# Performance work log

Hardware: AMD Instinct MI355X
Metric: run time of the kernel (lower is better)

The kernel has to match this reference:

```python
import jax, jax.numpy as jnp
import numpy as np
import math

T = 120      # frame_num == audio_len == max_seq_len
D = 64       # hidden_layer_size
H = 2        # n_head
DH = D // H
DFF = 2 * D
DOUT = 31
PERIOD = 10
EPS = 1e-5
NEG = -1e9
SCALE = 1.0 / math.sqrt(DH)
SLOPES = (1.0 / 16.0, 1.0 / 256.0)  # ALiBi slopes for n_head=2


def _pe():
    # PeriodicPositionalEncoding: sinusoid over one period, tiled
    pos = jnp.arange(PERIOD, dtype=jnp.float32)[:, None]
    div = jnp.exp(jnp.arange(0, D, 2, dtype=jnp.float32) * (-math.log(10000.0) / D))
    s, c = jnp.sin(pos * div), jnp.cos(pos * div)
    pe = jnp.stack([s, c], axis=-1).reshape(PERIOD, D)  # interleave sin/cos
    return jnp.tile(pe, (T // PERIOD + 1, 1))[:T]


def _alibi_mask():
    # causal mask + ALiBi bias: alibi[i,j] = -slope * floor((i-j)/period) for j<=i
    slopes = jnp.array(SLOPES, dtype=jnp.float32)
    i = jnp.arange(T)[:, None]
    j = jnp.arange(T)[None, :]
    rel = ((i - j) // PERIOD).astype(jnp.float32)
    return jnp.where(j <= i, -slopes[:, None, None] * rel, NEG)  # [H,T,T]


def _ln(x, g, b):
    m = x.mean(-1, keepdims=True)
    v = ((x - m) ** 2).mean(-1, keepdims=True)
    return (x - m) / jnp.sqrt(v + EPS) * g + b


def setup_inputs() -> dict:
    key = jax.random.key(0)
    ks = iter(jax.random.split(key, 32))
    n = lambda shape, s=0.05: jax.random.normal(next(ks), shape, dtype=jnp.float32) * s
    inp = {
        'audio': jax.random.normal(next(ks), (1, T, 1024), dtype=jnp.float32),
        'W_audio': n((D, 1024)), 'b_audio': n((D,)),
        'obj_W': n((D, 5)),
        'Wq': n((D, D)), 'bq': n((D,)), 'Wk': n((D, D)), 'bk': n((D,)),
        'Wv': n((D, D)), 'bv': n((D,)), 'Wo': n((D, D)), 'bo': n((D,)),
        'Wv2': n((D, D)), 'bv2': n((D,)), 'Wo2': n((D, D)), 'bo2': n((D,)),
        'g1': jnp.ones((D,)), 'be1': jnp.zeros((D,)),
        'g2': jnp.ones((D,)), 'be2': jnp.zeros((D,)),
        'g3': jnp.ones((D,)), 'be3': jnp.zeros((D,)),
        'W1': n((DFF, D)), 'c1': n((DFF,)), 'W2': n((D, DFF)), 'c2': n((D,)),
        'Wr': n((DOUT, D)), 'br': n((DOUT,)), 'Wm': n((D, DOUT)), 'bm': n((D,)),
    }
    return inp


def _forward(audio, W_audio, b_audio, obj_W, Wq, bq, Wk, bk, Wv, bv, Wo, bo,
             Wv2, bv2, Wo2, bo2, g1, be1, g2, be2, g3, be3,
             W1, c1, W2, c2, Wr, br, Wm, bm):
    mem = audio[0] @ W_audio.T + b_audio          # [S,D], S == T
    style = obj_W[:, 0]                            # obj_vector @ [1,0,0,0,0]
    pe = _pe()
    mask = _alibi_mask()
    slopes = jnp.array(SLOPES, dtype=jnp.float32)
    jarr = jnp.arange(T)

    # enc_dec_mask leaves exactly one memory key per target row (anti-diagonal
    # from the end); the feedback row t at step t always attends memory[-1],
    # so its cross-attn output is just the projected value of the last frame.
    cross_last = (mem[-1] @ Wv2.T + bv2) @ Wo2.T + bo2  # [D]

    def step(emb, t):
        # decode only the last row (row t) of the growing sequence; 1-layer
        # post-norm decoder => row t depends only on input rows 0..t.
        x = emb + pe                                 # PPE over prefix
        xq = jnp.take(x, t, axis=0)                  # [D]
        q = (xq @ Wq.T + bq).reshape(H, DH)
        k = (x @ Wk.T + bk).reshape(T, H, DH)
        v = (x @ Wv.T + bv).reshape(T, H, DH)
        bias = jnp.where(jarr <= t,
                         -slopes[:, None] * ((t - jarr) // PERIOD).astype(jnp.float32),
                         NEG)                        # [H,T]
        sc = jnp.einsum('hd,shd->hs', q, k) * SCALE + bias
        a = jax.nn.softmax(sc, axis=-1)
        sa = jnp.einsum('hs,shd->hd', a, v).reshape(D) @ Wo.T + bo
        h1 = _ln(xq + sa, g1, be1)
        h2 = _ln(h1 + cross_last, g2, be2)
        h3 = _ln(h2 + jax.nn.relu(h2 @ W1.T + c1) @ W2.T + c2, g3, be3)
        new = (h3 @ Wr.T + br) @ Wm.T + bm + style   # vertice_map(vertice_map_r(.)) + style
        emb = jax.lax.dynamic_update_slice(emb, new[None, :], (t + 1, 0))
        return emb, None

    emb0 = jnp.zeros((T, D), audio.dtype).at[0].set(style)
    emb, _ = jax.lax.scan(step, emb0, jnp.arange(T - 1))

    # final full-length decode (last loop iteration of the torch module)
    x = emb + pe
    q = (x @ Wq.T + bq).reshape(T, H, DH)
    k = (x @ Wk.T + bk).reshape(T, H, DH)
    v = (x @ Wv.T + bv).reshape(T, H, DH)
    sc = jnp.einsum('thd,shd->hts', q, k) * SCALE + mask
    a = jax.nn.softmax(sc, axis=-1)
    sa = jnp.einsum('hts,shd->thd', a, v).reshape(T, D) @ Wo.T + bo
    h1 = _ln(x + sa, g1, be1)
    # at length T with S == T the enc_dec_mask aligns target row j <-> memory row j
    cross = (mem @ Wv2.T + bv2) @ Wo2.T + bo2
    h2 = _ln(h1 + cross, g2, be2)
    h3 = _ln(h2 + jax.nn.relu(h2 @ W1.T + c1) @ W2.T + c2, g3, be3)
    return (h3 @ Wr.T + br)[None]                    # [1,T,31]


def reference(audio, W_audio, b_audio, obj_W, Wq, bq, Wk, bk, Wv, bv, Wo, bo,
              Wv2, bv2, Wo2, bo2, g1, be1, g2, be2, g3, be3,
              W1, c1, W2, c2, Wr, br, Wm, bm):
    return _forward(audio, W_audio, b_audio, obj_W, Wq, bq, Wk, bk, Wv, bv, Wo, bo,
                    Wv2, bv2, Wo2, bo2, g1, be1, g2, be2, g3, be3,
                    W1, c1, W2, c2, Wr, br, Wm, bm)
```

## Files before the change

kernel.cpp:

```cpp
#include <hip/hip_runtime.h>

typedef unsigned short u16;
typedef unsigned int   u32;
typedef _Float16 f16;
typedef f16 h2 __attribute__((ext_vector_type(2)));
typedef f16 h4 __attribute__((ext_vector_type(4)));
typedef f16 h8 __attribute__((ext_vector_type(8)));

#define T_    120
#define D_    64
#define DOUT_ 31
#define KROW_ 68
#define VROW_ 132
#define EROW_ 68

#if defined(__has_builtin)
#if __has_builtin(__builtin_amdgcn_fdot2)
#define DOT2(a,b,c) __builtin_amdgcn_fdot2((a),(b),(c),false)
#endif
#endif
#ifndef DOT2
#define DOT2(a,b,c) ((float)(a).x*(float)(b).x + ((float)(a).y*(float)(b).y + (c)))
#endif
#define SHV(x,i,j) __builtin_shufflevector((x),(x),(i),(j))

__device__ __forceinline__ h2 pk(float a, float b){
#if defined(__has_builtin) && __has_builtin(__builtin_amdgcn_cvt_pkrtz)
  return __builtin_bit_cast(h2, __builtin_amdgcn_cvt_pkrtz(a, b));
#else
  h2 r; r.x = (f16)a; r.y = (f16)b; return r;
#endif
}
__device__ __forceinline__ u16 f2h16(float x){
  f16 v = (f16)x; u16 r; __builtin_memcpy(&r, &v, 2); return r;
}
__device__ __forceinline__ float fast_rcp(float x){
#if defined(__has_builtin) && __has_builtin(__builtin_amdgcn_rcpf)
  return __builtin_amdgcn_rcpf(x);
#else
  return 1.f / x;
#endif
}
#define WSYNC() do{ __asm__ __volatile__("" ::: "memory"); __builtin_amdgcn_wave_barrier(); }while(0)

__device__ __forceinline__ float dpp_sum(float x){
  int t;
  t = __builtin_amdgcn_update_dpp(0, __float_as_int(x), 0x111, 0xf, 0xf, true); x += __int_as_float(t);
  t = __builtin_amdgcn_update_dpp(0, __float_as_int(x), 0x112, 0xf, 0xf, true); x += __int_as_float(t);
  t = __builtin_amdgcn_update_dpp(0, __float_as_int(x), 0x114, 0xf, 0xf, true); x += __int_as_float(t);
  t = __builtin_amdgcn_update_dpp(0, __float_as_int(x), 0x118, 0xf, 0xf, true); x += __int_as_float(t);
  t = __builtin_amdgcn_update_dpp(0, __float_as_int(x), 0x142, 0xf, 0xf, true); x += __int_as_float(t);
  t = __builtin_amdgcn_update_dpp(0, __float_as_int(x), 0x143, 0xf, 0xf, true); x += __int_as_float(t);
  return __int_as_float(__builtin_amdgcn_readlane(__float_as_int(x), 63));
}
__device__ __forceinline__ float dpp_max_pos(float x){
  int t;
  t = __builtin_amdgcn_update_dpp(0, __float_as_int(x), 0x111, 0xf, 0xf, true); x = fmaxf(x, __int_as_float(t));
  t = __builtin_amdgcn_update_dpp(0, __float_as_int(x), 0x112, 0xf, 0xf, true); x = fmaxf(x, __int_as_float(t));
  t = __builtin_amdgcn_update_dpp(0, __float_as_int(x), 0x114, 0xf, 0xf, true); x = fmaxf(x, __int_as_float(t));
  t = __builtin_amdgcn_update_dpp(0, __float_as_int(x), 0x118, 0xf, 0xf, true); x = fmaxf(x, __int_as_float(t));
  t = __builtin_amdgcn_update_dpp(0, __float_as_int(x), 0x142, 0xf, 0xf, true); x = fmaxf(x, __int_as_float(t));
  t = __builtin_amdgcn_update_dpp(0, __float_as_int(x), 0x143, 0xf, 0xf, true); x = fmaxf(x, __int_as_float(t));
  return __int_as_float(__builtin_amdgcn_readlane(__float_as_int(x), 63));
}
__device__ __forceinline__ float pe_val(int row, int i){
  const float coef = -0.28782313662425574f;
  int p = row % 10;
  float dv  = __expf((float)(i >> 1) * coef);
  float ang = (float)p * dv;
  return (i & 1) ? __cosf(ang) : __sinf(ang);
}
__device__ __forceinline__ void loadrow32(h2* dst, const float* row){
  #pragma unroll
  for (int r = 0; r < 16; ++r){
    float4 f = ((const float4*)row)[r];
    dst[2*r]   = pk(f.x, f.y);
    dst[2*r+1] = pk(f.z, f.w);
  }
}

__global__ __launch_bounds__(128, 1) void k_scan(
    const float* __restrict__ audio,
    const float* __restrict__ Wa, const float* __restrict__ ba,
    const float* __restrict__ Wv2, const float* __restrict__ bv2,
    const float* __restrict__ Wo2, const float* __restrict__ bo2,
    const float* __restrict__ objW,
    const float* __restrict__ Wq, const float* __restrict__ bq,
    const float* __restrict__ Wk, const float* __restrict__ bk,
    const float* __restrict__ Wv, const float* __restrict__ bv,
    const float* __restrict__ Wo, const float* __restrict__ bo,
    const float* __restrict__ g1, const float* __restrict__ be1,
    const float* __restrict__ g2, const float* __restrict__ be2,
    const float* __restrict__ g3, const float* __restrict__ be3,
    const float* __restrict__ W1, const float* __restrict__ c1,
    const float* __restrict__ W2, const float* __restrict__ c2,
    const float* __restrict__ Wm, const float* __restrict__ br,
    const float* __restrict__ bm, const float* __restrict__ Wr,
    u16* __restrict__ xw16, u16* __restrict__ Kw16, u16* __restrict__ Vw16)
{
  __shared__ __align__(16) f16 KcS[128*KROW_];
  __shared__ __align__(16) f16 VcS[D_*VROW_];
  __shared__ __align__(16) f16 xwS[T_*D_];
  __shared__ __align__(16) f16 EcS[64*EROW_];
  __shared__ __align__(16) f16 sch[256];
  __shared__ __align__(16) f16 xh[64], qh[64], h2h[64], h3h[64];
  __shared__ __align__(16) f16 at2h[64];
  __shared__ __align__(16) f16 fsh[128];
  __shared__ float pP0[64], pP1[64];
  __shared__ float ivP[2];
  __shared__ float pe_tab[640];

  const int tid = threadIdx.x;
  const int i = tid & 63;
  const int hh = tid >> 6;
  const bool w1w = hh != 0;

  h2 A[32], B[32], C[32], D[32], G[32];
  float biasA=0.f, biasB=0.f, bo_r=0.f, c1r=0.f, c2_r=0.f, cls_r=0.f;
  float g1r=0.f,b1r=0.f,g2r=0.f,b2r=0.f;
  float mg_r=0.f, u_r=0.f;
  float x_r;

  {
    float* ash = (float*)KcS;
    float* wrL = ((float*)KcS) + 1024;
    float* MsL = (float*)VcS;
    float* msh = (float*)xwS;
    float* tsh = ((float*)xwS) + 64;
    float* WmL = ((float*)xwS) + 128;
    #pragma unroll 4
    for (int idx = tid; idx < 1024; idx += 128) ash[idx] = audio[119*1024 + idx];
    #pragma unroll 4
    for (int idx = tid; idx < 1984; idx += 128){ wrL[idx] = Wr[idx]; WmL[idx] = Wm[idx]; }
    __syncthreads();
    #pragma clang loop unroll(disable)
    for (int d = hh*32; d < hh*32 + 32; ++d){
      const float4* row = (const float4*)(Wa + d*1024);
      float acc = 0.f;
      #pragma unroll
      for (int m = 0; m < 4; ++m){
        float4 wp = row[i + 64*m];
        int j = 4*(i + 64*m);
        acc += wp.x*ash[j] + wp.y*ash[j+1] + wp.z*ash[j+2] + wp.w*ash[j+3];
      }
      acc = dpp_sum(acc);
      if (i == 0) msh[d] = acc + ba[d];
    }
    #pragma clang loop unroll(disable)
    for (int od = tid; od < 1024; od += 128){
      int d = od >> 4, q = od & 15;
      float4 acc4 = make_float4(0.f, 0.f, 0.f, 0.f);
      #pragma unroll 4
      for (int j = 0; j < 31; ++j){
        float4 w4 = ((const float4*)(wrL + j*64))[q];
        float s = WmL[d*31 + j];
        acc4.x += s*w4.x; acc4.y += s*w4.y; acc4.z += s*w4.z; acc4.w += s*w4.w;
      }
      ((float4*)(MsL + d*64))[q] = acc4;
    }
    __syncthreads();
    if (tid < 64){
      const float4* r1 = (const float4*)(Wv2 + tid*64);
      float a = bv2[tid];
      #pragma unroll 4
      for (int j = 0; j < 16; ++j){ float4 p = r1[j]; a += p.x*msh[4*j] + p.y*msh[4*j+1] + p.z*msh[4*j+2] + p.w*msh[4*j+3]; }
      tsh[tid] = a;
    }
    __syncthreads();
    {
      const float4* r2 = (const float4*)(Wo2 + i*64);
      float c = bo2[i];
      #pragma unroll 4
      for (int j = 0; j < 16; ++j){ float4 p = r2[j]; c += p.x*tsh[4*j] + p.y*tsh[4*j+1] + p.z*tsh[4*j+2] + p.w*tsh[4*j+3]; }
      cls_r = c;
    }
    {
      const float4* mr  = (const float4*)(MsL + i*64);
      const float4* gv  = (const float4*)g3;
      const float4* b3v = (const float4*)be3;
      u32* erow = (u32*)(EcS + i*EROW_);
      float mg = 0.f, mb = 0.f;
      #pragma unroll 4
      for (int r = 0; r < 16; ++r){
        float4 f = mr[r], g = gv[r], b = b3v[r];
        float e0 = f.x*g.x, e1 = f.y*g.y, e2 = f.z*g.z, e3 = f.w*g.w;
        erow[2*r]   = __builtin_bit_cast(u32, pk(e0, e1));
        erow[2*r+1] = __builtin_bit_cast(u32, pk(e2, e3));
        mg += (e0+e1)+(e2+e3);
        mb += f.x*b.x + f.y*b.y + f.z*b.z + f.w*b.w;
      }
      mg_r = mg;
      float bsum = 0.f;
      #pragma unroll 4
      for (int j = 0; j < 31; ++j) bsum += WmL[i*31 + j] * br[j];
      u_r = bm[i] + bsum + objW[i*5] + mb;
    }
    __syncthreads();
  }

  {
    const int qi = hh*32 + (i & 31);
    if (i < 32){ loadrow32(A, Wq + qi*64); biasA = bq[qi]; }
    else       { loadrow32(A, Wk + qi*64); biasA = bk[qi]; }
    loadrow32(B, Wv + qi*64);  biasB = bv[qi];
    loadrow32(C, Wo + i*64);
    loadrow32(D, W1 + (hh*64 + i)*64);
    loadrow32(G, W2 + i*128 + hh*64);
    c1r = c1[hh*64 + i]; c2_r = c2[i]; bo_r = bo[i];
    g1r = g1[i]; b1r = be1[i]; g2r = g2[i]; b2r = be2[i];
  }
  { u32* p = (u32*)KcS; for (int idx = tid; idx < 128*KROW_/2; idx += 128) p[idx] = 0; }
  { u32* p = (u32*)VcS; for (int idx = tid; idx < D_*VROW_/2;  idx += 128) p[idx] = 0; }
  #pragma clang loop unroll(disable)
  for (int idx = tid; idx < 640; idx += 128) pe_tab[idx] = pe_val(idx >> 6, idx & 63);
  {
    float x0 = objW[i*5] + pe_val(0, i);
    x_r = x0;
    xh[i] = (f16)x0;
    if (w1w) xwS[i] = (f16)x0;
  }
  __syncthreads();

  int pp = 1;
  const float slope = hh ? 0.00390625f : 0.0625f;
  for (int t = 0; t < T_-1; ++t){
    float e0r, e1r;
    h8 xr[8];
    {
      const h8* xv = (const h8*)xh;
      #pragma unroll
      for (int r = 0; r < 8; ++r) xr[r] = xv[r];
      float a0=biasA,a1=0.f,a2=0.f,a3=0.f;
      #pragma unroll
      for (int r = 0; r < 8; ++r){
        h8 x = xr[r];
        a0 = DOT2(A[4*r+0], SHV(x,0,1), a0);
        a1 = DOT2(A[4*r+1], SHV(x,2,3), a1);
        a2 = DOT2(A[4*r+2], SHV(x,4,5), a2);
        a3 = DOT2(A[4*r+3], SHV(x,6,7), a3);
      }
      float qk = (a0+a1)+(a2+a3);
      f16* dst = (i < 32) ? (qh + hh*32 + i) : (KcS + t*KROW_ + hh*32 + (i - 32));
      *dst = (f16)qk;
    }
    WSYNC();
    {
      if (i < 32){
        float v0=biasB,v1=0.f,v2=0.f,v3=0.f;
        #pragma unroll
        for (int r = 0; r < 8; ++r){
          h8 x = xr[r];
          v0 = DOT2(B[4*r+0], SHV(x,0,1), v0); v1 = DOT2(B[4*r+1], SHV(x,2,3), v1);
          v2 = DOT2(B[4*r+2], SHV(x,4,5), v2); v3 = DOT2(B[4*r+3], SHV(x,6,7), v3);
        }
        VcS[(hh*32 + i)*VROW_ + t] = (f16)((v0+v1)+(v2+v3));
      }
      const int j = i;
      const h8* qv = (const h8*)(qh + hh*32);
      const h4* k0 = (const h4*)(KcS + j*KROW_ + hh*32);
      const h4* k1 = (const h4*)(KcS + (j+64)*KROW_ + hh*32);
      float d0a=0.f,d0b=0.f,d1a=0.f,d1b=0.f;
      #pragma unroll
      for (int r = 0; r < 4; ++r){
        h8 q = qv[r];
        h4 ka = k0[2*r], kb = k0[2*r+1], kc = k1[2*r], kd = k1[2*r+1];
        d0a = DOT2(SHV(ka,0,1), SHV(q,0,1), d0a);
        d0b = DOT2(SHV(ka,2,3), SHV(q,2,3), d0b);
        d0a = DOT2(SHV(kb,0,1), SHV(q,4,5), d0a);
        d0b = DOT2(SHV(kb,2,3), SHV(q,6,7), d0b);
        d1a = DOT2(SHV(kc,0,1), SHV(q,0,1), d1a);
        d1b = DOT2(SHV(kc,2,3), SHV(q,2,3), d1b);
        d1a = DOT2(SHV(kd,0,1), SHV(q,4,5), d1a);
        d1b = DOT2(SHV(kd,2,3), SHV(q,6,7), d1b);
      }
      float d0 = d0a + d0b, d1 = d1a + d1b;
      int r0 = (t - j) / 10, r1 = (t - j - 64) / 10;
      float s0 = d0*0.17677669529663687f - slope*(float)r0;
      float s1 = d1*0.17677669529663687f - slope*(float)r1;
      e0r = (j      <= t) ? __expf(fminf(s0, 8.f)) : 0.f;
      e1r = (j + 64 <= t) ? __expf(fminf(s1, 8.f)) : 0.f;
      sch[hh*128 + j]      = (f16)e0r;
      sch[hh*128 + j + 64] = (f16)e1r;
    }
    WSYNC();
    {
      float den = dpp_sum(e0r + e1r);
      float inv_w = fast_rcp(den);
      if (i == 0) ivP[hh] = inv_w;
      const int l5 = i & 31;
      const int d  = hh*32 + l5;
      const int co = (i & 32) ? 64 : 0;
      const h8* av = (const h8*)(sch + hh*128 + co);
      const h4* vv = (const h4*)(VcS + d*VROW_ + co);
      float p0=0.f,p1=0.f,p2=0.f,p3=0.f;
      #pragma unroll
      for (int r = 0; r < 8; ++r){
        h8 a = av[r];
        h4 va = vv[2*r], vb = vv[2*r+1];
        p0 = DOT2(SHV(va,0,1), SHV(a,0,1), p0);
        p1 = DOT2(SHV(va,2,3), SHV(a,2,3), p1);
        p2 = DOT2(SHV(vb,0,1), SHV(a,4,5), p2);
        p3 = DOT2(SHV(vb,2,3), SHV(a,6,7), p3);
      }
      float p = (p0+p1)+(p2+p3);
      p += __shfl_xor(p, 32, 64);
      at2h[hh*32 + l5] = (f16)p;
    }
    __syncthreads();
    float h2v;
    {
      float inv0 = ivP[0], inv1 = ivP[1];
      const h8* pv = (const h8*)at2h;
      float l0=0.f,l1=0.f,q0=0.f,q1=0.f;
      #pragma unroll
      for (int r = 0; r < 4; ++r){
        h8 x = pv[r];
        l0 = DOT2(C[4*r+0], SHV(x,0,1), l0); l1 = DOT2(C[4*r+1], SHV(x,2,3), l1);
        l0 = DOT2(C[4*r+2], SHV(x,4,5), l0); l1 = DOT2(C[4*r+3], SHV(x,6,7), l1);
      }
      #pragma unroll
      for (int r = 4; r < 8; ++r){
        h8 x = pv[r];
        q0 = DOT2(C[4*r+0], SHV(x,0,1), q0); q1 = DOT2(C[4*r+1], SHV(x,2,3), q1);
        q0 = DOT2(C[4*r+2], SHV(x,4,5), q0); q1 = DOT2(C[4*r+3], SHV(x,6,7), q1);
      }
      float sa = bo_r + inv0*(l0+l1) + inv1*(q0+q1);
      float y = x_r + sa;
      float s = dpp_sum(y), s2 = dpp_sum(y*y);
      float m = s*(1.f/64.f), var = fmaxf(s2*(1.f/64.f) - m*m, 0.f);
      float h1 = (y - m)*rsqrtf(var + 1e-5f)*g1r + b1r;
      float z = h1 + cls_r;
      float sz = dpp_sum(z), sz2 = dpp_sum(z*z);
      float mz = sz*(1.f/64.f), vz = fmaxf(sz2*(1.f/64.f) - mz*mz, 0.f);
      h2v = (z - mz)*rsqrtf(vz + 1e-5f)*g2r + b2r;
      h2h[i] = (f16)h2v;
      WSYNC();
      const h8* hv = (const h8*)h2h;
      float a0=c1r, a1=0.f, a2=0.f, a3=0.f;
      #pragma unroll
      for (int r = 0; r < 8; ++r){
        h8 x = hv[r];
        a0 = DOT2(D[4*r+0], SHV(x,0,1), a0);
        a1 = DOT2(D[4*r+1], SHV(x,2,3), a1);
        a2 = DOT2(D[4*r+2], SHV(x,4,5), a2);
        a3 = DOT2(D[4*r+3], SHV(x,6,7), a3);
      }
      fsh[hh*64 + i] = (f16)fmaxf((a0+a1)+(a2+a3), 0.f);
      WSYNC();
      const h8* fv = (const h8*)(fsh + hh*64);
      float f0=0.f, f1=0.f, f2=0.f, f3=0.f;
      #pragma unroll
      for (int r = 0; r < 8; ++r){
        h8 x = fv[r];
        f0 = DOT2(G[4*r+0], SHV(x,0,1), f0);
        f1 = DOT2(G[4*r+1], SHV(x,2,3), f1);
        f2 = DOT2(G[4*r+2], SHV(x,4,5), f2);
        f3 = DOT2(G[4*r+3], SHV(x,6,7), f3);
      }
      float* pP = hh ? pP1 : pP0;
      pP[i] = (f0+f1)+(f2+f3);
    }
    __syncthreads();
    {
      float y3 = h2v + c2_r + pP0[i] + pP1[i];
      h3h[i] = (f16)y3;
      WSYNC();
      const h8* yv3 = (const h8*)h3h;
      h8 yr[8];
      #pragma unroll
      for (int r = 0; r < 8; ++r) yr[r] = yv3[r];
      const h4* Ev = (const h4*)(EcS + i*EROW_);
      h4 er[16];
      #pragma unroll
      for (int r = 0; r < 16; ++r) er[r] = Ev[r];
      float s3 = dpp_sum(y3), s32 = dpp_sum(y3*y3);
      float m3 = s3*(1.f/64.f), v3 = fmaxf(s32*(1.f/64.f) - m3*m3, 0.f);
      float invs = rsqrtf(v3 + 1e-5f);
      float m0=0.f, m1=0.f, m2=0.f, mm3=0.f;
      #pragma unroll
      for (int r = 0; r < 8; ++r){
        h8 x = yr[r];
        m0 = DOT2(SHV(er[2*r],0,1),   SHV(x,0,1), m0);
        m1 = DOT2(SHV(er[2*r],2,3),   SHV(x,2,3), m1);
        m2 = DOT2(SHV(er[2*r+1],0,1), SHV(x,4,5), m2);
        mm3 = DOT2(SHV(er[2*r+1],2,3), SHV(x,6,7), mm3);
      }
      float xn = ((m0+m1)+(m2+mm3))*invs + (u_r - m3*invs*mg_r) + pe_tab[pp*64 + i];
      x_r = xn;
      xh[i] = (f16)xn;
      if (w1w) xwS[(t+1)*64 + i] = (f16)xn;
    }
    WSYNC();
    pp = (pp == 9) ? 0 : pp + 1;
  }
  {
    const h8* xv = (const h8*)xh;
    h8 xr[8];
    #pragma unroll
    for (int r = 0; r < 8; ++r) xr[r] = xv[r];
    if (i < 32){
      float v0=biasB,v1=0.f,v2=0.f,v3=0.f;
      #pragma unroll
      for (int r = 0; r < 8; ++r){
        h8 x = xr[r];
        v0 = DOT2(B[4*r+0], SHV(x,0,1), v0);
        v1 = DOT2(B[4*r+1], SHV(x,2,3), v1);
        v2 = DOT2(B[4*r+2], SHV(x,4,5), v2);
        v3 = DOT2(B[4*r+3], SHV(x,6,7), v3);
      }
      Vw16[119*64 + hh*32 + i] = f2h16((v0+v1)+(v2+v3));
    } else {
      float k0=biasA,k1=0.f,k2=0.f,k3=0.f;
      #pragma unroll
      for (int r = 0; r < 8; ++r){
        h8 x = xr[r];
        k0 = DOT2(A[4*r+0], SHV(x,0,1), k0);
        k1 = DOT2(A[4*r+1], SHV(x,2,3), k1);
        k2 = DOT2(A[4*r+2], SHV(x,4,5), k2);
        k3 = DOT2(A[4*r+3], SHV(x,6,7), k3);
      }
      Kw16[119*64 + hh*32 + (i-32)] = f2h16((k0+k1)+(k2+k3));
    }
  }
  __syncthreads();
  {
    const u16* kc = (const u16*)KcS;
    const u16* vc = (const u16*)VcS;
    #pragma unroll 4
    for (int idx = tid; idx < 119*64; idx += 128){
      int t_ = idx >> 6, d = idx & 63;
      Kw16[idx] = kc[t_*KROW_ + d];
      Vw16[idx] = vc[d*VROW_ + t_];
    }
    const u32* xs32 = (const u32*)xwS;
    #pragma unroll 4
    for (int idx = tid; idx < T_*D_/2; idx += 128) ((u32*)xw16)[idx] = xs32[idx];
  }
}

__global__ __launch_bounds__(128) void k_final(
    const float* __restrict__ audio,
    const float* __restrict__ Wa, const float* __restrict__ ba,
    const float* __restrict__ Wv2, const float* __restrict__ bv2,
    const float* __restrict__ Wo2, const float* __restrict__ bo2,
    const float* __restrict__ Wq, const float* __restrict__ bq,
    const float* __restrict__ Wo, const float* __restrict__ bo,
    const float* __restrict__ g1, const float* __restrict__ be1,
    const float* __restrict__ g2, const float* __restrict__ be2,
    const float* __restrict__ g3, const float* __restrict__ be3,
    const float* __restrict__ W1, const float* __restrict__ c1,
    const float* __restrict__ W2, const float* __restrict__ c2,
    const float* __restrict__ Wr, const float* __restrict__ br,
    const u16* __restrict__ xw16, const u16* __restrict__ Kw16, const u16* __restrict__ Vw16,
    float* __restrict__ out)
{
  __shared__ float ash[1024], msh[64], tsh[64], crs[64];
  __shared__ float xs[64], qs[64], at[64], h2s[64], h3s[64], fs[128], sc[256];
  const int irow = blockIdx.x, tid = threadIdx.x;
  const f16* xp = (const f16*)xw16;
  const f16* kp = (const f16*)Kw16;
  const f16* vp = (const f16*)Vw16;
  for (int idx = tid; idx < 1024; idx += 128) ash[idx] = audio[irow*1024 + idx];
  if (tid < 64) xs[tid] = (float)xp[irow*64 + tid];
  __syncthreads();
  {
    const int w = tid >> 6, lane = tid & 63;
    for (int d = w*32; d < w*32 + 32; ++d){
      const float4* row = (const float4*)(Wa + d*1024);
      float acc = 0.f;
      #pragma unroll
      for (int m = 0; m < 4; ++m){
        float4 wp = row[lane + 64*m];
        int j = 4*(lane + 64*m);
        acc += wp.x*ash[j] + wp.y*ash[j+1] + wp.z*ash[j+2] + wp.w*ash[j+3];
      }
      acc = dpp_sum(acc);
      if (lane == 0) msh[d] = acc + ba[d];
    }
  }
  __syncthreads();
  if (tid < 64){
    const float4* r1 = (const float4*)(Wv2 + tid*64);
    float a = bv2[tid];
    #pragma unroll
    for (int j = 0; j < 16; ++j){ float4 p = r1[j]; a += p.x*msh[4*j] + p.y*msh[4*j+1] + p.z*msh[4*j+2] + p.w*msh[4*j+3]; }
    tsh[tid] = a;
  }
  __syncthreads();
  if (tid < 64){
    const float4* r2 = (const float4*)(Wo2 + tid*64);
    float c = bo2[tid];
    #pragma unroll
    for (int j = 0; j < 16; ++j){ float4 p = r2[j]; c += p.x*tsh[4*j] + p.y*tsh[4*j+1] + p.z*tsh[4*j+2] + p.w*tsh[4*j+3]; }
    crs[tid] = c;
  }
  __syncthreads();
  if (tid < 64){
    const float4* wr_ = (const float4*)(Wq + tid*64);
    float acc = bq[tid];
    #pragma unroll
    for (int j = 0; j < 16; ++j){ float4 w = wr_[j]; acc += w.x*xs[4*j] + w.y*xs[4*j+1] + w.z*xs[4*j+2] + w.w*xs[4*j+3]; }
    qs[tid] = acc;
  }
  __syncthreads();
  {
    const int h = tid >> 6, j = tid & 63;
    const float* qh_ = qs + h*32;
    float d0 = 0.f, d1 = 0.f;
    const h4* k0 = (const h4*)(kp + j*64 + h*32);
    #pragma unroll
    for (int w = 0; w < 8; ++w){
      h4 p = k0[w];
      d0 += (float)p.x*qh_[4*w] + (float)p.y*qh_[4*w+1] + (float)p.z*qh_[4*w+2] + (float)p.w*qh_[4*w+3];
    }
    if (j < 56){
      const h4* k1 = (const h4*)(kp + (j+64)*64 + h*32);
      #pragma unroll
      for (int w = 0; w < 8; ++w){
        h4 p = k1[w];
        d1 += (float)p.x*qh_[4*w] + (float)p.y*qh_[4*w+1] + (float)p.z*qh_[4*w+2] + (float)p.w*qh_[4*w+3];
      }
    }
    const float slope = h ? 0.00390625f : 0.0625f;
    float s0 = (j      <= irow) ? d0*0.17677669529663687f - slope*(float)((irow-j)/10)    : -1e30f;
    float s1 = (j + 64 <= irow) ? d1*0.17677669529663687f - slope*(float)((irow-j-64)/10) : -1e30f;
    float m = dpp_max_pos(fmaxf(s0, s1) + 16384.f) - 16384.f;
    float e0 = (j      <= irow) ? __expf(s0 - m) : 0.f;
    float e1 = (j + 64 <= irow) ? __expf(s1 - m) : 0.f;
    float inv = 1.f / dpp_sum(e0 + e1);
    sc[h*128 + j]      = e0*inv;
    sc[h*128 + j + 64] = e1*inv;
  }
  __syncthreads();
  if (tid < 64){
    const float* a = sc + (tid >> 5)*128;
    float a0=0.f,a1=0.f,a2=0.f,a3=0.f;
    #pragma unroll
    for (int jj = 0; jj < 30; ++jj){
      a0 += a[4*jj]   * (float)vp[(4*jj)*64   + tid];
      a1 += a[4*jj+1] * (float)vp[(4*jj+1)*64 + tid];
      a2 += a[4*jj+2] * (float)vp[(4*jj+2)*64 + tid];
      a3 += a[4*jj+3] * (float)vp[(4*jj+3)*64 + tid];
    }
    at[tid] = (a0+a1)+(a2+a3);
  }
  __syncthreads();
  if (tid < 64){
    const float4* orow = (const float4*)(Wo + tid*64);
    float acc = bo[tid];
    #pragma unroll
    for (int w = 0; w < 16; ++w){ float4 p = orow[w]; acc += p.x*at[4*w] + p.y*at[4*w+1] + p.z*at[4*w+2] + p.w*at[4*w+3]; }
    float y = xs[tid] + acc;
    float s = dpp_sum(y), s2 = dpp_sum(y*y);
    float m = s*(1.f/64.f), var = fmaxf(s2*(1.f/64.f) - m*m, 0.f);
    float h1 = (y - m)*rsqrtf(var + 1e-5f)*g1[tid] + be1[tid];
    float z = h1 + crs[tid];
    float sz = dpp_sum(z), sz2 = dpp_sum(z*z);
    float mz = sz*(1.f/64.f), vz = fmaxf(sz2*(1.f/64.f) - mz*mz, 0.f);
    h2s[tid] = (z - mz)*rsqrtf(vz + 1e-5f)*g2[tid] + be2[tid];
  }
  __syncthreads();
  {
    const float4* w1r = (const float4*)(W1 + tid*64);
    float acc = c1[tid];
    #pragma unroll
    for (int w = 0; w < 16; ++w){ float4 p = w1r[w]; acc += p.x*h2s[4*w] + p.y*h2s[4*w+1] + p.z*h2s[4*w+2] + p.w*h2s[4*w+3]; }
    fs[tid] = fmaxf(acc, 0.f);
  }
  __syncthreads();
  if (tid < 64){
    const float4* w2r = (const float4*)(W2 + tid*128);
    float acc = c2[tid];
    #pragma unroll
    for (int w = 0; w < 32; ++w){ float4 p = w2r[w]; acc += p.x*fs[4*w] + p.y*fs[4*w+1] + p.z*fs[4*w+2] + p.w*fs[4*w+3]; }
    float y = h2s[tid] + acc;
    float s = dpp_sum(y), s2 = dpp_sum(y*y);
    float m = s*(1.f/64.f), var = fmaxf(s2*(1.f/64.f) - m*m, 0.f);
    h3s[tid] = (y - m)*rsqrtf(var + 1e-5f)*g3[tid] + be3[tid];
  }
  __syncthreads();
  if (tid < DOUT_){
    const float4* rr = (const float4*)(Wr + tid*64);
    float acc = br[tid];
    #pragma unroll
    for (int w = 0; w < 16; ++w){ float4 p = rr[w]; acc += p.x*h3s[4*w] + p.y*h3s[4*w+1] + p.z*h3s[4*w+2] + p.w*h3s[4*w+3]; }
    out[irow*DOUT_ + tid] = acc;
  }
}

extern "C" void kernel_launch(void* const* d_in, const int* in_sizes, int n_in,
                              void* d_out, int out_size, void* d_ws, size_t ws_size,
                              hipStream_t stream){
  const float* audio=(const float*)d_in[0];
  const float* Wa   =(const float*)d_in[1];
  const float* ba   =(const float*)d_in[2];
  const float* objW =(const float*)d_in[3];
  const float* Wq   =(const float*)d_in[4];
  const float* bq   =(const float*)d_in[5];
  const float* Wk   =(const float*)d_in[6];
  const float* bk   =(const float*)d_in[7];
  const float* Wv   =(const float*)d_in[8];
  const float* bv   =(const float*)d_in[9];
  const float* Wo   =(const float*)d_in[10];
  const float* bo   =(const float*)d_in[11];
  const float* Wv2  =(const float*)d_in[12];
  const float* bv2  =(const float*)d_in[13];
  const float* Wo2  =(const float*)d_in[14];
  const float* bo2  =(const float*)d_in[15];
  const float* g1   =(const float*)d_in[16];
  const float* be1  =(const float*)d_in[17];
  const float* g2   =(const float*)d_in[18];
  const float* be2  =(const float*)d_in[19];
  const float* g3   =(const float*)d_in[20];
  const float* be3  =(const float*)d_in[21];
  const float* W1   =(const float*)d_in[22];
  const float* c1   =(const float*)d_in[23];
  const float* W2   =(const float*)d_in[24];
  const float* c2   =(const float*)d_in[25];
  const float* Wr   =(const float*)d_in[26];
  const float* br   =(const float*)d_in[27];
  const float* Wm   =(const float*)d_in[28];
  const float* bm   =(const float*)d_in[29];

  u16* xw16 = (u16*)d_ws;
  u16* Kw16 = xw16 + 7680;
  u16* Vw16 = Kw16 + 7680;
  float* out = (float*)d_out;

  k_scan <<<dim3(1),   dim3(128), 0, stream>>>(audio, Wa, ba, Wv2, bv2, Wo2, bo2,
                                               objW, Wq, bq, Wk, bk, Wv, bv, Wo, bo,
                                               g1, be1, g2, be2, g3, be3,
                                               W1, c1, W2, c2, Wm, br, bm, Wr,
                                               xw16, Kw16, Vw16);
  k_final<<<dim3(120), dim3(128), 0, stream>>>(audio, Wa, ba, Wv2, bv2, Wo2, bo2,
                                               Wq, bq, Wo, bo, g1, be1, g2, be2, g3, be3,
                                               W1, c1, W2, c2, Wr, br,
                                               xw16, Kw16, Vw16, out);
}
```

Baseline: 393.8 us.

## Keep E matrix in registers and split Wo projection per head wave

Stores the fused Wm·diag(g3) matrix E in per-thread registers instead of LDS, which removes 16 LDS vector loads per step. The Wo output projection is split by head, so each wave multiplies only its own 32-wide attention slice, with the softmax normalizer folded in locally. Partial sums are exchanged through shared memory after the existing barrier, and the separate ivP broadcast is removed. This costs more registers (E adds 32 h2 while C drops to 16) and an extra wave-level sync, and it may raise register pressure.

```diff
diff --git a/kernel.cpp b/kernel.cpp
--- a/kernel.cpp
+++ b/kernel.cpp
@@ -12,7 +12,6 @@
 #define DOUT_ 31
 #define KROW_ 68
 #define VROW_ 132
-#define EROW_ 68
 
 #if defined(__has_builtin)
 #if __has_builtin(__builtin_amdgcn_fdot2)
@@ -73,6 +72,14 @@
 __device__ __forceinline__ void loadrow32(h2* dst, const float* row){
   #pragma unroll
   for (int r = 0; r < 16; ++r){
+    float4 f = ((const float4*)row)[r];
+    dst[2*r]   = pk(f.x, f.y);
+    dst[2*r+1] = pk(f.z, f.w);
+  }
+}
+__device__ __forceinline__ void loadrow16(h2* dst, const float* row){
+  #pragma unroll
+  for (int r = 0; r < 8; ++r){
     float4 f = ((const float4*)row)[r];
     dst[2*r]   = pk(f.x, f.y);
     dst[2*r+1] = pk(f.z, f.w);
@@ -101,13 +108,12 @@
   __shared__ __align__(16) f16 KcS[128*KROW_];
   __shared__ __align__(16) f16 VcS[D_*VROW_];
   __shared__ __align__(16) f16 xwS[T_*D_];
-  __shared__ __align__(16) f16 EcS[64*EROW_];
   __shared__ __align__(16) f16 sch[256];
   __shared__ __align__(16) f16 xh[64], qh[64], h2h[64], h3h[64];
-  __shared__ __align__(16) f16 at2h[64];
+  __shared__ __align__(16) f16 at0h[32], at1h[32];
   __shared__ __align__(16) f16 fsh[128];
+  __shared__ float saP0[64], saP1[64];
   __shared__ float pP0[64], pP1[64];
-  __shared__ float ivP[2];
   __shared__ float pe_tab[640];
 
   const int tid = threadIdx.x;
@@ -115,7 +121,7 @@
   const int hh = tid >> 6;
   const bool w1w = hh != 0;
 
-  h2 A[32], B[32], C[32], D[32], G[32];
+  h2 A[32], B[32], C[16], D[32], G[32], E[32];
   float biasA=0.f, biasB=0.f, bo_r=0.f, c1r=0.f, c2_r=0.f, cls_r=0.f;
   float g1r=0.f,b1r=0.f,g2r=0.f,b2r=0.f;
   float mg_r=0.f, u_r=0.f;
@@ -178,14 +184,13 @@
       const float4* mr  = (const float4*)(MsL + i*64);
       const float4* gv  = (const float4*)g3;
       const float4* b3v = (const float4*)be3;
-      u32* erow = (u32*)(EcS + i*EROW_);
       float mg = 0.f, mb = 0.f;
       #pragma unroll 4
       for (int r = 0; r < 16; ++r){
         float4 f = mr[r], g = gv[r], b = b3v[r];
         float e0 = f.x*g.x, e1 = f.y*g.y, e2 = f.z*g.z, e3 = f.w*g.w;
-        erow[2*r]   = __builtin_bit_cast(u32, pk(e0, e1));
-        erow[2*r+1] = __builtin_bit_cast(u32, pk(e2, e3));
+        E[2*r]   = pk(e0, e1);
+        E[2*r+1] = pk(e2, e3);
         mg += (e0+e1)+(e2+e3);
         mb += f.x*b.x + f.y*b.y + f.z*b.z + f.w*b.w;
       }
@@ -203,7 +208,7 @@
     if (i < 32){ loadrow32(A, Wq + qi*64); biasA = bq[qi]; }
     else       { loadrow32(A, Wk + qi*64); biasA = bk[qi]; }
     loadrow32(B, Wv + qi*64);  biasB = bv[qi];
-    loadrow32(C, Wo + i*64);
+    loadrow16(C, Wo + i*64 + hh*32);
     loadrow32(D, W1 + (hh*64 + i)*64);
     loadrow32(G, W2 + i*128 + hh*64);
     c1r = c1[hh*64 + i]; c2_r = c2[i]; bo_r = bo[i];
@@ -286,7 +291,6 @@
     {
       float den = dpp_sum(e0r + e1r);
       float inv_w = fast_rcp(den);
-      if (i == 0) ivP[hh] = inv_w;
       const int l5 = i & 31;
       const int d  = hh*32 + l5;
       const int co = (i & 32) ? 64 : 0;
@@ -304,27 +308,26 @@
       }
       float p = (p0+p1)+(p2+p3);
       p += __shfl_xor(p, 32, 64);
-      at2h[hh*32 + l5] = (f16)p;
+      f16* ath = hh ? at1h : at0h;
+      ath[l5] = (f16)p;
+      WSYNC();
+      const h8* pv = (const h8*)ath;
+      float w0a=0.f,w1a=0.f,w2a=0.f,w3a=0.f;
+      #pragma unroll
+      for (int r = 0; r < 4; ++r){
+        h8 x = pv[r];
+        w0a = DOT2(C[4*r+0], SHV(x,0,1), w0a);
+        w1a = DOT2(C[4*r+1], SHV(x,2,3), w1a);
+        w2a = DOT2(C[4*r+2], SHV(x,4,5), w2a);
+        w3a = DOT2(C[4*r+3], SHV(x,6,7), w3a);
+      }
+      float* saP = hh ? saP1 : saP0;
+      saP[i] = inv_w * ((w0a+w1a)+(w2a+w3a));
     }
     __syncthreads();
     float h2v;
     {
-      float inv0 = ivP[0], inv1 = ivP[1];
-      const h8* pv = (const h8*)at2h;
-      float l0=0.f,l1=0.f,q0=0.f,q1=0.f;
-      #pragma unroll
-      for (int r = 0; r < 4; ++r){
-        h8 x = pv[r];
-        l0 = DOT2(C[4*r+0], SHV(x,0,1), l0); l1 = DOT2(C[4*r+1], SHV(x,2,3), l1);
-        l0 = DOT2(C[4*r+2], SHV(x,4,5), l0); l1 = DOT2(C[4*r+3], SHV(x,6,7), l1);
-      }
-      #pragma unroll
-      for (int r = 4; r < 8; ++r){
-        h8 x = pv[r];
-        q0 = DOT2(C[4*r+0], SHV(x,0,1), q0); q1 = DOT2(C[4*r+1], SHV(x,2,3), q1);
-        q0 = DOT2(C[4*r+2], SHV(x,4,5), q0); q1 = DOT2(C[4*r+3], SHV(x,6,7), q1);
-      }
-      float sa = bo_r + inv0*(l0+l1) + inv1*(q0+q1);
+      float sa = bo_r + saP0[i] + saP1[i];
       float y = x_r + sa;
       float s = dpp_sum(y), s2 = dpp_sum(y*y);
       float m = s*(1.f/64.f), var = fmaxf(s2*(1.f/64.f) - m*m, 0.f);
@@ -369,10 +372,6 @@
       h8 yr[8];
       #pragma unroll
       for (int r = 0; r < 8; ++r) yr[r] = yv3[r];
-      const h4* Ev = (const h4*)(EcS + i*EROW_);
-      h4 er[16];
-      #pragma unroll
-      for (int r = 0; r < 16; ++r) er[r] = Ev[r];
       float s3 = dpp_sum(y3), s32 = dpp_sum(y3*y3);
       float m3 = s3*(1.f/64.f), v3 = fmaxf(s32*(1.f/64.f) - m3*m3, 0.f);
       float invs = rsqrtf(v3 + 1e-5f);
@@ -380,10 +379,10 @@
       #pragma unroll
       for (int r = 0; r < 8; ++r){
         h8 x = yr[r];
-        m0 = DOT2(SHV(er[2*r],0,1),   SHV(x,0,1), m0);
-        m1 = DOT2(SHV(er[2*r],2,3),   SHV(x,2,3), m1);
-        m2 = DOT2(SHV(er[2*r+1],0,1), SHV(x,4,5), m2);
-        mm3 = DOT2(SHV(er[2*r+1],2,3), SHV(x,6,7), mm3);
+        m0 = DOT2(E[4*r+0], SHV(x,0,1), m0);
+        m1 = DOT2(E[4*r+1], SHV(x,2,3), m1);
+        m2 = DOT2(E[4*r+2], SHV(x,4,5), m2);
+        mm3 = DOT2(E[4*r+3], SHV(x,6,7), mm3);
       }
       float xn = ((m0+m1)+(m2+mm3))*invs + (u_r - m3*invs*mg_r) + pe_tab[pp*64 + i];
       x_r = xn;
```

Measured after the change: 397.6 us. No clear change (+1.0%).
